# Optimization experiments

Hardware: AMD Instinct MI355X
Metric: run time of the kernel (lower is better)

## Reference

```python
import jax, jax.numpy as jnp
import numpy as np
import math

# Dims: d_model=192, expand=2 -> d_inner=d_ssm=384, headdim=64 -> nheads=6,
# d_state=128, K=4 scan directions, ngroups=1 (directions fused into state dim).
D_MODEL = 192
D_STATE = 128
D_CONV = 3
EXPAND = 2
HEADDIM = 64
CHUNK = 256
D_INNER = EXPAND * D_MODEL          # 384
D_SSM = D_INNER                     # default d_ssm (d_mlp == 0)
NHEADS = D_SSM // HEADDIM           # 6
K = 4                               # scan directions
HTOT = K * NHEADS                   # 24 heads in the fused scan
NSTATE = K * D_STATE                # 512 fused state dim (ngroups=1)
CONV_BC = 2 * D_STATE + NHEADS      # 262
B, H, W = 2, 64, 64


def _dwconv(x, w, b):
    # x: (B,C,H,W), w: (C,1,k,k) depthwise, SAME padding ((k-1)//2)
    y = jax.lax.conv_general_dilated(
        x, w, (1, 1), [(1, 1), (1, 1)],
        feature_group_count=x.shape[1],
        dimension_numbers=('NCHW', 'OIHW', 'NCHW'))
    return y + b[None, :, None, None]


def _ssd(x, dt_raw, A_logs, Bm, Cm, Ds, dt_bias):
    # Mamba2 chunked selective scan (dt_softplus=True, default dt_limit).
    # x: (b,l,h,p)  dt_raw: (b,l,h)  Bm,Cm: (b,l,n) with ngroups=1
    A = -jnp.exp(A_logs)                              # (h,)
    dt = jax.nn.softplus(dt_raw + dt_bias)            # (b,l,h)
    b, l, h, p = x.shape
    n = Bm.shape[-1]
    nc = l // CHUNK
    xc = x.reshape(b, nc, CHUNK, h, p)
    dtc = dt.reshape(b, nc, CHUNK, h)
    Bc = Bm.reshape(b, nc, CHUNK, n)
    Cc = Cm.reshape(b, nc, CHUNK, n)
    dA = dtc * A                                      # (b,nc,cs,h)
    acum = jnp.cumsum(dA, axis=2)
    # intra-chunk (causal, attention-like)
    a_t = jnp.transpose(acum, (0, 1, 3, 2))           # (b,nc,h,cs)
    diff = a_t[..., :, None] - a_t[..., None, :]      # (b,nc,h,i,j)
    causal = jnp.tril(jnp.ones((CHUNK, CHUNK), bool))
    Lmat = jnp.where(causal, jnp.exp(diff), 0.0)
    CB = jnp.einsum('bcin,bcjn->bcij', Cc, Bc)        # (b,nc,i,j)
    M = CB[:, :, None] * Lmat * jnp.transpose(dtc, (0, 1, 3, 2))[:, :, :, None, :]
    y = jnp.einsum('bchij,bcjhp->bcihp', M, xc)
    # chunk-final states
    decay_end = jnp.exp(acum[:, :, -1:, :] - acum)    # (b,nc,cs,h)
    states = jnp.einsum('bcjh,bcjn,bcjhp->bchpn', decay_end * dtc, Bc, xc)
    chunk_decay = jnp.exp(acum[:, :, -1, :])          # (b,nc,h)

    def step(S, inp):
        st, dec = inp
        return S * dec[:, :, None, None] + st, S

    S0 = jnp.zeros((b, h, p, n), x.dtype)
    _, prev = jax.lax.scan(step, S0, (jnp.moveaxis(states, 1, 0),
                                      jnp.moveaxis(chunk_decay, 1, 0)))
    prev = jnp.moveaxis(prev, 0, 1)                   # (b,nc,h,p,n)
    y = y + jnp.einsum('bcih,bcin,bchpn->bcihp', jnp.exp(acum), Cc, prev)
    y = y + xc * Ds[:, None]                          # D skip connection
    return y.reshape(b, l, h, p)


def _branch(u, u_cross, W_skip, W_xs, W_bcdt, conv_xs_w, conv_xs_b,
            conv_bc_w, conv_bc_b, dt_bias, A_logs, Ds, norm_w, W_out):
    Bb, Hh, Ww, _ = u.shape
    L = Hh * Ww
    z = (u @ W_skip).reshape(Bb, L, D_SSM)            # gate (d_mlp == 0)
    xs = jnp.transpose(u @ W_xs, (0, 3, 1, 2))        # (B,d_ssm,H,W)
    xs = jax.nn.silu(_dwconv(xs, conv_xs_w, conv_xs_b))
    bc = jnp.transpose(u_cross @ W_bcdt, (0, 3, 1, 2))
    bc = jax.nn.silu(_dwconv(bc, conv_bc_w, conv_bc_b))
    xbc = jnp.concatenate([xs, bc], axis=1)           # (B,646,H,W)
    C = xbc.shape[1]
    v = xbc.reshape(Bb, C, L)                         # HW raster
    vt = jnp.transpose(xbc, (0, 1, 3, 2)).reshape(Bb, C, L)  # WH raster
    hw = jnp.stack([v, vt], axis=1)                   # (B,2,C,L)
    xbcdt = jnp.concatenate([hw, jnp.flip(hw, axis=-1)], axis=1)  # (B,4,C,L)
    xp = xbcdt[:, :, :D_SSM]
    Bp = xbcdt[:, :, D_SSM:D_SSM + D_STATE]
    Cp = xbcdt[:, :, D_SSM + D_STATE:D_SSM + 2 * D_STATE]
    dtp = xbcdt[:, :, D_SSM + 2 * D_STATE:]
    x = xp.reshape(Bb, K * D_SSM, L).transpose(0, 2, 1).reshape(Bb, L, HTOT, HEADDIM)
    Bm = Bp.reshape(Bb, NSTATE, L).transpose(0, 2, 1)
    Cm = Cp.reshape(Bb, NSTATE, L).transpose(0, 2, 1)
    dt = dtp.reshape(Bb, HTOT, L).transpose(0, 2, 1)
    y = _ssd(x, dt, A_logs, Bm, Cm, Ds, dt_bias)      # (B,L,24,64)
    y = y.reshape(Bb, L, K, D_SSM)
    out_y = y[:, :, 0]
    inv_y = jnp.flip(y[:, :, 2:4], axis=1)            # (B,L,2,d_ssm)
    wh_y = y[:, :, 1].reshape(Bb, Ww, Hh, D_SSM).transpose(0, 2, 1, 3).reshape(Bb, L, D_SSM)
    invwh_y = inv_y[:, :, 1].reshape(Bb, Ww, Hh, D_SSM).transpose(0, 2, 1, 3).reshape(Bb, L, D_SSM)
    yf = out_y + inv_y[:, :, 0] + wh_y + invwh_y
    # gated RMSNorm (norm_before_gate=False, group_size == d_ssm)
    g = yf * jax.nn.silu(z)
    g = g * jax.lax.rsqrt(jnp.mean(g * g, axis=-1, keepdims=True) + 1e-5) * norm_w
    return (g @ W_out).reshape(Bb, Hh, Ww, D_MODEL)


def setup_inputs():
    key = jax.random.key(0)
    ks = jax.random.split(key, 16)
    f = lambda i, s: jax.random.normal(ks[i], s, jnp.float32)
    sc = 0.02
    dt = jnp.exp(jax.random.uniform(ks[10], (NHEADS,)) *
                 (math.log(0.1) - math.log(0.001)) + math.log(0.001))
    dt = jnp.maximum(dt, 1e-4)
    inv_dt = dt + jnp.log(-jnp.expm1(-dt))
    A = jax.random.uniform(ks[11], (NHEADS,), minval=1.0, maxval=16.0)
    return {
        'u1': f(0, (B, H, W, D_MODEL)),
        'u2': f(1, (B, H, W, D_MODEL)),
        'u2_cat_u1': f(2, (B, H, W, D_MODEL)),
        'u1_cat_u2': f(3, (B, H, W, D_MODEL)),
        'W_skip': f(4, (D_MODEL, D_SSM)) * sc,
        'W_xs': f(5, (D_MODEL, D_SSM)) * sc,
        'W_bcdt': f(6, (D_MODEL, CONV_BC)) * sc,
        'conv_xs_w': f(7, (D_SSM, 1, D_CONV, D_CONV)) * sc,
        'conv_xs_b': jnp.zeros((D_SSM,), jnp.float32),
        'conv_bc_w': f(8, (CONV_BC, 1, D_CONV, D_CONV)) * sc,
        'conv_bc_b': jnp.zeros((CONV_BC,), jnp.float32),
        'dt_bias': jnp.tile(inv_dt, K),
        'A_logs': jnp.tile(jnp.log(A), K),
        'Ds': jnp.ones((HTOT,), jnp.float32),
        'norm_w': jnp.ones((D_SSM,), jnp.float32),
        'W_out': f(9, (D_SSM, D_MODEL)) * sc,
    }


def reference(u1, u2, u2_cat_u1, u1_cat_u2, W_skip, W_xs, W_bcdt,
              conv_xs_w, conv_xs_b, conv_bc_w, conv_bc_b,
              dt_bias, A_logs, Ds, norm_w, W_out):
    args = (W_skip, W_xs, W_bcdt, conv_xs_w, conv_xs_b, conv_bc_w,
            conv_bc_b, dt_bias, A_logs, Ds, norm_w, W_out)
    out1 = _branch(u1, u2_cat_u1, *args)
    out2 = _branch(u2, u1_cat_u2, *args)
    return out1, out2
```

## Files before the change

### kernel.cpp

```cpp
#include <hip/hip_runtime.h>
#include <hip/hip_bf16.h>

#define DEV __device__ __forceinline__

static constexpr int LL   = 4096;
static constexpr int GG   = 4;
static constexpr int CBC  = 262;

typedef float f32x4  __attribute__((ext_vector_type(4)));
typedef short bf16x8 __attribute__((ext_vector_type(8)));
typedef short bf16x4v __attribute__((ext_vector_type(4)));
typedef short bf16x2 __attribute__((ext_vector_type(2)));

DEV int map_l(int s, int k) {
    int m = (k & 2) ? (4095 - s) : s;
    if (k & 1) m = ((m & 63) << 6) | (m >> 6);
    return m;
}
DEV float silu_f(float x) { return x / (1.f + __expf(-x)); }
DEV short f2bf(float f) {
    union { __hip_bfloat16 h; short s; } u;
    u.h = __float2bfloat16(f);
    return u.s;
}
DEV float bf2f(short s) {
    return __uint_as_float(((unsigned)(unsigned short)s) << 16);
}
DEV bf16x8 pack8(float4 a, float4 b) {
    bf16x8 r;
    r[0]=f2bf(a.x); r[1]=f2bf(a.y); r[2]=f2bf(a.z); r[3]=f2bf(a.w);
    r[4]=f2bf(b.x); r[5]=f2bf(b.y); r[6]=f2bf(b.z); r[7]=f2bf(b.w);
    return r;
}
DEV bf16x8 load8u(const __hip_bfloat16* p) {
    bf16x4v lo = *(const bf16x4v*)p;
    bf16x4v hi = *(const bf16x4v*)(p + 4);
    bf16x8 r;
    r[0]=lo[0]; r[1]=lo[1]; r[2]=lo[2]; r[3]=lo[3];
    r[4]=hi[0]; r[5]=hi[1]; r[6]=hi[2]; r[7]=hi[3];
    return r;
}
DEV void store16(__hip_bfloat16* p, const float* v) {
    bf16x8 a, b;
    #pragma unroll
    for (int e = 0; e < 8; ++e) { a[e] = f2bf(v[e]); b[e] = f2bf(v[8+e]); }
    *(bf16x8*)p = a;
    *((bf16x8*)p + 1) = b;
}
DEV void storeT(float v, float* p) { *p = v; }
DEV void storeT(float v, __hip_bfloat16* p) { *p = __float2bfloat16(v); }

__global__ void sentinel_k(float* out) { out[0] = 1e30f; }

__global__ void wt_all_k(const float* __restrict__ W_skip, const float* __restrict__ W_xs,
                         const float* __restrict__ W_bcdt, const float* __restrict__ W_out,
                         const float* __restrict__ norm_w, __hip_bfloat16* __restrict__ Wt)
{
    int idx = blockIdx.x * 256 + threadIdx.x;
    if (idx < 73728) {
        int n = idx / 192, k = idx - n * 192;
        Wt[idx] = __float2bfloat16(W_skip[(size_t)k * 384 + n]);
    } else if (idx < 147456) {
        int r = idx - 73728;
        int n = r / 192, k = r - n * 192;
        Wt[idx] = __float2bfloat16(W_xs[(size_t)k * 384 + n]);
    } else if (idx < 208896) {
        int r = idx - 147456;
        int n = r / 192, k = r - n * 192;
        Wt[idx] = __float2bfloat16(n < 262 ? W_bcdt[(size_t)k * 262 + n] : 0.f);
    } else if (idx < 282624) {
        int r = idx - 208896;
        int n = r / 384, k = r - n * 384;
        Wt[idx] = __float2bfloat16(W_out[(size_t)k * 192 + n] * norm_w[k]);
    }
}

template<int MODE, typename AT, typename OutT>
DEV void mgemm_body(const AT* __restrict__ A0, const AT* __restrict__ A1,
                    const __hip_bfloat16* __restrict__ Wt, OutT* __restrict__ C,
                    OutT* __restrict__ C2, int N, int Kd, int i0, int j0)
{
    int t = threadIdx.x;
    int w = t >> 6, lane = t & 63;
    int lr = lane & 15, kq = lane >> 4;
    const AT* arow[2];
    #pragma unroll
    for (int a = 0; a < 2; ++a) {
        int grow = i0 + w * 32 + a * 16 + lr;
        const AT* Ap = (grow < 8192) ? A0 : A1;
        arow[a] = Ap + (size_t)(grow & 8191) * Kd;
    }
    f32x4 acc[2][4] = {};
    for (int k0 = 0; k0 < Kd; k0 += 32) {
        int kb = k0 + kq * 8;
        bf16x8 af[2];
        #pragma unroll
        for (int a = 0; a < 2; ++a) {
            if constexpr (sizeof(AT) == 4)
                af[a] = pack8(*(const float4*)(arow[a] + kb), *(const float4*)(arow[a] + kb + 4));
            else
                af[a] = *(const bf16x8*)(arow[a] + kb);
        }
        #pragma unroll
        for (int b = 0; b < 4; ++b) {
            int n = j0 + b * 16 + lr;
            bf16x8 bfr = *(const bf16x8*)(Wt + (size_t)n * Kd + kb);
            #pragma unroll
            for (int a = 0; a < 2; ++a)
                acc[a][b] = __builtin_amdgcn_mfma_f32_16x16x32_bf16(af[a], bfr, acc[a][b], 0, 0, 0);
        }
    }
    #pragma unroll
    for (int a = 0; a < 2; ++a)
        #pragma unroll
        for (int b = 0; b < 4; ++b)
            #pragma unroll
            for (int r = 0; r < 4; ++r) {
                int row = i0 + w * 32 + a * 16 + kq * 4 + r;
                int col = j0 + b * 16 + lr;
                float v = acc[a][b][r];
                if constexpr (MODE == 0) {
                    if (col < N) storeT(v, &C[(size_t)row * N + col]);
                } else if constexpr (MODE == 1) {
                    if (col < N) storeT(silu_f(v), &C[(size_t)row * N + col]);
                } else {
                    if (col < 384) storeT(silu_f(v), &C[(size_t)row * 384 + col]);
                    else           storeT(v, &C2[(size_t)row * 384 + col - 384]);
                }
            }
}

__global__ __launch_bounds__(256) void mgemm_in_k(
    const float* __restrict__ u1, const float* __restrict__ u2,
    const float* __restrict__ u21, const float* __restrict__ u12,
    const __hip_bfloat16* __restrict__ Wt_skip, const __hip_bfloat16* __restrict__ Wt_bcdt,
    __hip_bfloat16* __restrict__ z_silu, __hip_bfloat16* __restrict__ pre_xs,
    __hip_bfloat16* __restrict__ pre_bc)
{
    int bid = blockIdx.x;
    if (bid < 1536) {
        mgemm_body<2, float, __hip_bfloat16>(u1, u2, Wt_skip, z_silu, pre_xs,
                                             768, 192, (bid / 12) * 128, (bid % 12) * 64);
    } else {
        int b = bid - 1536;
        mgemm_body<0, float, __hip_bfloat16>(u21, u12, Wt_bcdt, pre_bc, nullptr,
                                             CBC, 192, (b / 5) * 128, (b % 5) * 64);
    }
}

template<int STRIDE>
DEV void conv16(const __hip_bfloat16* __restrict__ pre, const float* __restrict__ cw,
                const float* __restrict__ cbia, int g, int h0, int w0, int chb,
                float* smem, float (*wsm)[9], float* bsm, int t)
{
    if (t < 144) wsm[t / 9][t % 9] = cw[(chb + t / 9) * 9 + t % 9];
    if (t < 16)  bsm[t] = cbia[chb + t];
    for (int i = t; i < 18 * 18 * 8; i += 256) {
        int cp = i & 7;
        int hw = i >> 3;
        int ww2 = hw % 18, hh = hw / 18;
        int gh = h0 - 1 + hh, gw = w0 - 1 + ww2;
        float v0 = 0.f, v1 = 0.f;
        if ((unsigned)gh < 64u && (unsigned)gw < 64u) {
            bf16x2 pv = *(const bf16x2*)(pre + ((size_t)g * LL + gh * 64 + gw) * STRIDE + chb + cp * 2);
            v0 = bf2f(pv[0]); v1 = bf2f(pv[1]);
        }
        smem[(hh * 18 + ww2) * 17 + cp * 2]     = v0;
        smem[(hh * 18 + ww2) * 17 + cp * 2 + 1] = v1;
    }
    __syncthreads();
    int h = t >> 4, w2 = t & 15;
    float out[16];
    #pragma unroll
    for (int ch = 0; ch < 16; ++ch) {
        float acc = bsm[ch];
        #pragma unroll
        for (int dy = 0; dy < 3; ++dy)
            #pragma unroll
            for (int dx = 0; dx < 3; ++dx)
                acc += smem[((h + dy) * 18 + (w2 + dx)) * 17 + ch] * wsm[ch][dy * 3 + dx];
        out[ch] = silu_f(acc);
    }
    __syncthreads();
    #pragma unroll
    for (int ch = 0; ch < 16; ++ch)
        smem[(h * 17 + w2) * 17 + ch] = out[ch];
    __syncthreads();
}

__global__ __launch_bounds__(256) void prep_k(
    const __hip_bfloat16* __restrict__ pre_bc, const float* __restrict__ cbw,
    const float* __restrict__ cbb, const __hip_bfloat16* __restrict__ pre_xs,
    const float* __restrict__ cxw, const float* __restrict__ cxb,
    const float* __restrict__ dt_bias, const float* __restrict__ A_logs,
    __hip_bfloat16* __restrict__ Bt, __hip_bfloat16* __restrict__ Cs,
    __hip_bfloat16* __restrict__ Bs, __hip_bfloat16* __restrict__ XtG,
    float* __restrict__ dt_arr, float* __restrict__ ac_arr,
    float* __restrict__ cdecay)
{
    __shared__ float smem[18 * 18 * 17];
    __shared__ float wsm[16][9];
    __shared__ float bsm[16];
    __shared__ float wsum[4];
    int bid = blockIdx.x;
    int t = threadIdx.x;
    if (bid < 2048) {
        int nt = bid & 31;
        int rest = bid >> 5;
        int wt = rest & 3, ht2 = (rest >> 2) & 3, g = rest >> 4;
        int h0 = ht2 * 16, w0 = wt * 16;
        int kd = nt >> 3, ch0 = (nt & 7) * 16;
        conv16<262>(pre_bc, cbw, cbb, g, h0, w0, ch0, smem, wsm, bsm, t);
        int pc = t >> 4, q = t & 15;
        int n = nt * 16 + pc;
        __hip_bfloat16* rowp = Bt + ((size_t)g * 512 + n) * 4096;
        float v[16];
        if (kd == 0) {
            #pragma unroll
            for (int e = 0; e < 16; ++e) v[e] = smem[(q * 17 + e) * 17 + pc];
            store16(rowp + (h0 + q) * 64 + w0, v);
        } else if (kd == 1) {
            #pragma unroll
            for (int e = 0; e < 16; ++e) v[e] = smem[(e * 17 + q) * 17 + pc];
            store16(rowp + (w0 + q) * 64 + h0, v);
        } else if (kd == 2) {
            #pragma unroll
            for (int e = 0; e < 16; ++e) v[e] = smem[(q * 17 + 15 - e) * 17 + pc];
            store16(rowp + 4095 - (h0 + q) * 64 - w0 - 15, v);
        } else {
            #pragma unroll
            for (int e = 0; e < 16; ++e) v[e] = smem[((15 - e) * 17 + q) * 17 + pc];
            store16(rowp + 4095 - (w0 + q) * 64 - h0 - 15, v);
        }
    } else if (bid < 4096) {
        int b2 = bid - 2048;
        int ct = b2 & 31;
        int rest = b2 >> 5;
        int wt = rest & 3, ht2 = (rest >> 2) & 3, g = rest >> 4;
        int h0 = ht2 * 16, w0 = wt * 16;
        bool isB = ct >= 16;
        int ctl = ct & 15;
        int kd = ctl >> 3, ch0 = (ctl & 7) * 16;
        int chb = (isB ? 0 : 128) + ch0;
        conv16<262>(pre_bc, cbw, cbb, g, h0, w0, chb, smem, wsm, bsm, t);
        __hip_bfloat16* dst = isB ? Bs : Cs;
        int h = t >> 4, w2 = t & 15;
        int s = (kd == 0) ? (h0 + h) * 64 + (w0 + w2) : (w0 + w2) * 64 + (h0 + h);
        float v[16];
        #pragma unroll
        for (int e = 0; e < 16; ++e) v[e] = smem[(h * 17 + w2) * 17 + e];
        store16(dst + ((size_t)g * 4096 + s) * 256 + kd * 128 + ch0, v);
    } else if (bid < 5632) {
        int b3 = bid - 4096;
        int ht = b3 % 24;
        int gc = b3 / 24;
        int c = gc & 15, g = gc >> 4;
        int k = ht / 6, h = ht % 6;
        int s = c * 256 + t;
        int l = map_l(s, k);
        int ch = 256 + h;
        float acc = cbb[ch];
        int hh0 = l >> 6, ww0 = l & 63;
        #pragma unroll
        for (int dy = 0; dy < 3; ++dy) {
            int gh = hh0 + dy - 1;
            if ((unsigned)gh >= 64u) continue;
            #pragma unroll
            for (int dx = 0; dx < 3; ++dx) {
                int gw = ww0 + dx - 1;
                if ((unsigned)gw >= 64u) continue;
                acc += __bfloat162float(pre_bc[((size_t)g * LL + gh * 64 + gw) * 262 + ch]) *
                       cbw[ch * 9 + dy * 3 + dx];
            }
        }
        float raw = silu_f(acc) + dt_bias[ht];
        float dtv = raw > 20.f ? raw : log1pf(__expf(raw));
        float dA = dtv * (-__expf(A_logs[ht]));
        float v = dA;
        #pragma unroll
        for (int off = 1; off < 64; off <<= 1) {
            float u = __shfl_up(v, off);
            if ((t & 63) >= off) v += u;
        }
        if ((t & 63) == 63) wsum[t >> 6] = v;
        __syncthreads();
        float add = 0.f;
        #pragma unroll
        for (int w2 = 0; w2 < 3; ++w2)
            if (w2 < (t >> 6)) add += wsum[w2];
        float cum = v + add;
        size_t base = ((size_t)g * 24 + ht) * LL + s;
        dt_arr[base] = dtv;
        ac_arr[base] = cum;
        if (t == 255) cdecay[(g * 24 + ht) * 16 + c] = __expf(cum);
    } else {
        int b4 = bid - 5632;
        int pct = b4 % 24;
        int rest = b4 / 24;
        int wt = rest & 3, ht2 = (rest >> 2) & 3, g = rest >> 4;
        int h0 = ht2 * 16, w0 = wt * 16, pc0 = pct * 16;
        conv16<384>(pre_xs, cxw, cxb, g, h0, w0, pc0, smem, wsm, bsm, t);
        int pc = t >> 4, q = t & 15;
        float v[16];
        size_t rowbase;
        #pragma unroll
        for (int e = 0; e < 16; ++e) v[e] = smem[(q * 17 + e) * 17 + pc];
        rowbase = ((size_t)(g * 2 + 0) * 384 + pc0 + pc) * 4096;
        store16(XtG + rowbase + (h0 + q) * 64 + w0, v);
        #pragma unroll
        for (int e = 0; e < 16; ++e) v[e] = smem[(e * 17 + q) * 17 + pc];
        rowbase = ((size_t)(g * 2 + 1) * 384 + pc0 + pc) * 4096;
        store16(XtG + rowbase + (w0 + q) * 64 + h0, v);
    }
}

__global__ __launch_bounds__(256) void cbst_k(
    const __hip_bfloat16* __restrict__ Cs, const __hip_bfloat16* __restrict__ Bs,
    __hip_bfloat16* __restrict__ CBm,
    const __hip_bfloat16* __restrict__ XtG, const __hip_bfloat16* __restrict__ Bt,
    const float* __restrict__ dt_arr, const float* __restrict__ ac_arr,
    __hip_bfloat16* __restrict__ states)
{
    __shared__ float wsh[256];
    __shared__ short xw[64][264];
    int bid = blockIdx.x;
    int t = threadIdx.x;
    int w = t >> 6, lane = t & 63;
    int lr = lane & 15, kq = lane >> 4;
    if (bid < 256) {
        int jq = bid & 3;
        int gc = bid >> 2;
        int c = gc & 15, g = gc >> 4;
        const __hip_bfloat16* cg = Cs + (size_t)g * 4096 * 256;
        const __hip_bfloat16* bsg = Bs + (size_t)g * 4096 * 256;
        f32x4 acc[4][4] = {};
        for (int ks = 0; ks < 16; ++ks) {
            int n0 = ks * 32 + kq * 8;
            int kd = n0 >> 7, nn = n0 & 127;
            int col = ((kd & 1) << 7) + nn;
            bf16x8 bfr[4];
            #pragma unroll
            for (int jt = 0; jt < 4; ++jt) {
                int j = jq * 64 + jt * 16 + lr;
                int s = c * 256 + j;
                int row = (kd < 2) ? s : 4095 - s;
                bfr[jt] = *(const bf16x8*)(bsg + (size_t)row * 256 + col);
            }
            #pragma unroll
            for (int iq = 0; iq < 4; ++iq) {
                int i = (w * 4 + iq) * 16 + lr;
                int s = c * 256 + i;
                int row = (kd < 2) ? s : 4095 - s;
                bf16x8 af = *(const bf16x8*)(cg + (size_t)row * 256 + col);
                #pragma unroll
                for (int jt = 0; jt < 4; ++jt)
                    acc[iq][jt] = __builtin_amdgcn_mfma_f32_16x16x32_bf16(af, bfr[jt], acc[iq][jt], 0, 0, 0);
            }
        }
        __hip_bfloat16* ob = CBm + (size_t)gc * 65536;
        #pragma unroll
        for (int iq = 0; iq < 4; ++iq)
            #pragma unroll
            for (int jt = 0; jt < 4; ++jt)
                #pragma unroll
                for (int r = 0; r < 4; ++r) {
                    int i = (w * 4 + iq) * 16 + kq * 4 + r;
                    int j = jq * 64 + jt * 16 + lr;
                    ob[(size_t)i * 256 + j] = __float2bfloat16(acc[iq][jt][r]);
                }
        return;
    }
    int sb = bid - 256;
    int task = (sb & 7) * 384 + (sb >> 3);
    int ht = task % 24;
    int rest = task / 24;
    int nh = rest & 1;
    int gc = rest >> 1;
    int c = gc & 15, g = gc >> 4;
    int kd = ht / 6;
    bool rev = kd >= 2;
    int c0 = (ht % 6) * 64;
    int n0 = nh * 256;
    const float* dtp = dt_arr + ((size_t)g * 24 + ht) * LL + c * 256;
    const float* acp = ac_arr + ((size_t)g * 24 + ht) * LL + c * 256;
    float ac_last = acp[255];
    wsh[t] = __expf(ac_last - acp[t]) * dtp[t];
    __syncthreads();
    const __hip_bfloat16* xg = XtG + ((size_t)(g * 2 + (kd & 1)) * 384 + c0) * 4096;
    #pragma unroll
    for (int r8 = 0; r8 < 8; ++r8) {
        int id = t + 256 * r8;
        int p = id >> 5;
        int jc = (id & 31) * 8;
        bf16x8 xv;
        if (!rev) {
            xv = *(const bf16x8*)(xg + (size_t)p * 4096 + c * 256 + jc);
        } else {
            bf16x8 tmp = load8u(xg + (size_t)p * 4096 + 4088 - c * 256 - jc);
            #pragma unroll
            for (int e = 0; e < 8; ++e) xv[e] = tmp[7 - e];
        }
        bf16x8 o;
        #pragma unroll
        for (int e = 0; e < 8; ++e) o[e] = f2bf(bf2f(xv[e]) * wsh[jc + e]);
        *(bf16x8*)&xw[p][jc] = o;
    }
    __syncthreads();
    const __hip_bfloat16* btg = Bt + ((size_t)g * 512 + n0) * 4096;
    f32x4 acc[4][4] = {};
    for (int ks = 0; ks < 8; ++ks) {
        int j0 = ks * 32 + kq * 8;
        bf16x8 af[4];
        #pragma unroll
        for (int pt = 0; pt < 4; ++pt)
            af[pt] = *(const bf16x8*)&xw[pt * 16 + lr][j0];
        #pragma unroll
        for (int nt = 0; nt < 4; ++nt) {
            int nl = (w * 4 + nt) * 16 + lr;
            bf16x8 bv = *(const bf16x8*)(btg + (size_t)nl * 4096 + c * 256 + j0);
            #pragma unroll
            for (int pt = 0; pt < 4; ++pt)
                acc[pt][nt] = __builtin_amdgcn_mfma_f32_16x16x32_bf16(af[pt], bv, acc[pt][nt], 0, 0, 0);
        }
    }
    __hip_bfloat16* ob = states + ((size_t)gc * 24 + ht) * 32768 + n0;
    #pragma unroll
    for (int pt = 0; pt < 4; ++pt)
        #pragma unroll
        for (int nt = 0; nt < 4; ++nt)
            #pragma unroll
            for (int r = 0; r < 4; ++r) {
                int p = pt * 16 + kq * 4 + r;
                int nl = (w * 4 + nt) * 16 + lr;
                ob[(size_t)p * 512 + nl] = __float2bfloat16(acc[pt][nt][r]);
            }
}

__global__ void scan_k(__hip_bfloat16* __restrict__ states, const float* __restrict__ cdecay)
{
    int idx = blockIdx.x * 256 + threadIdx.x;
    int g = idx / 98304;
    int r = idx - g * 98304;
    int ht = r >> 12;
    int pn8 = (r & 4095) * 8;
    const float* cd = cdecay + (g * 24 + ht) * 16;
    __hip_bfloat16* base = states + ((size_t)g * 384 + ht) * 32768 + pn8;
    float S[8] = {};
    #pragma unroll
    for (int c2 = 0; c2 < 16; ++c2) {
        bf16x8* p = (bf16x8*)(base + (size_t)c2 * 786432);
        bf16x8 tmp = *p;
        bf16x8 o;
        float dec = cd[c2];
        #pragma unroll
        for (int e = 0; e < 8; ++e) {
            o[e] = f2bf(S[e]);
            S[e] = S[e] * dec + bf2f(tmp[e]);
        }
        *p = o;
    }
}

__global__ __launch_bounds__(256) void yk(
    const __hip_bfloat16* __restrict__ XtG, const __hip_bfloat16* __restrict__ Cs,
    const __hip_bfloat16* __restrict__ CBm, const __hip_bfloat16* __restrict__ prev,
    const float* __restrict__ dt_arr, const float* __restrict__ ac_arr,
    const float* __restrict__ Ds, __hip_bfloat16* __restrict__ y4)
{
    __shared__ float acs[256], dts[256], ejdt[256];
    __shared__ short xl[64][264];
    int task = (blockIdx.x & 7) * 192 + (blockIdx.x >> 3);
    int ht = task % 24;
    int gc = task / 24;
    int c = gc & 15, g = gc >> 4;
    int kd = ht / 6;
    bool rev = kd >= 2;
    int c0 = (ht % 6) * 64;
    int t = threadIdx.x;
    int w = t >> 6, lane = t & 63;
    int lr = lane & 15, kq = lane >> 4;
    size_t abase = ((size_t)g * 24 + ht) * LL + c * 256;
    float ac_own = ac_arr[abase + t];
    float dt_own = dt_arr[abase + t];
    acs[t] = ac_own;
    dts[t] = dt_own;
    float acb0 = __shfl(ac_own, (t & 63) & ~31);
    ejdt[t] = __expf(acb0 - ac_own) * dt_own;
    const __hip_bfloat16* xg = XtG + ((size_t)(g * 2 + (kd & 1)) * 384 + c0) * 4096;
    #pragma unroll
    for (int r8 = 0; r8 < 8; ++r8) {
        int id = t + 256 * r8;
        int p = id >> 5;
        int jc = (id & 31) * 8;
        bf16x8 xv;
        if (!rev) {
            xv = *(const bf16x8*)(xg + (size_t)p * 4096 + c * 256 + jc);
        } else {
            bf16x8 tmp = load8u(xg + (size_t)p * 4096 + 4088 - c * 256 - jc);
            #pragma unroll
            for (int e = 0; e < 8; ++e) xv[e] = tmp[7 - e];
        }
        *(bf16x8*)&xl[p][jc] = xv;
    }
    __syncthreads();
    const __hip_bfloat16* cbb = CBm + (size_t)gc * 65536;
    const __hip_bfloat16* cg = Cs + (size_t)g * 4096 * 256;
    f32x4 acc[4][4] = {};
    const __hip_bfloat16* pv = prev + ((size_t)gc * 24 + ht) * 32768;
    auto ld2 = [&](int ns, bf16x8* afq, bf16x8* pb) {
        int n0 = ns * 32 + kq * 8;
        int kd2 = n0 >> 7, nn = n0 & 127;
        int col = ((kd2 & 1) << 7) + nn;
        #pragma unroll
        for (int q = 0; q < 4; ++q) {
            int i = (w + 4 * q) * 16 + lr;
            int s = c * 256 + i;
            int row = (kd2 < 2) ? s : 4095 - s;
            afq[q] = *(const bf16x8*)(cg + (size_t)row * 256 + col);
        }
        #pragma unroll
        for (int pt = 0; pt < 4; ++pt)
            pb[pt] = *(const bf16x8*)(pv + (size_t)(pt * 16 + lr) * 512 + n0);
    };
    auto fma2 = [&](bf16x8* afq, bf16x8* pb) {
        #pragma unroll
        for (int q = 0; q < 4; ++q)
            #pragma unroll
            for (int pt = 0; pt < 4; ++pt)
                acc[q][pt] = __builtin_amdgcn_mfma_f32_16x16x32_bf16(afq[q], pb[pt], acc[q][pt], 0, 0, 0);
    };
    {
        bf16x8 afA[4], pbA[4], afB[4], pbB[4];
        ld2(0, afA, pbA);
        #pragma unroll
        for (int ns = 0; ns < 16; ns += 2) {
            if (ns + 1 < 16) ld2(ns + 1, afB, pbB);
            fma2(afA, pbA);
            if (ns + 2 < 16) ld2(ns + 2, afA, pbA);
            fma2(afB, pbB);
        }
    }
    #pragma unroll
    for (int q = 0; q < 4; ++q)
        #pragma unroll
        for (int r = 0; r < 4; ++r) {
            float er = __expf(acs[(w + 4 * q) * 16 + kq * 4 + r]);
            #pragma unroll
            for (int pt = 0; pt < 4; ++pt) acc[q][pt][r] *= er;
        }
    float aci_q[4];
    #pragma unroll
    for (int q = 0; q < 4; ++q) aci_q[q] = acs[(w + 4 * q) * 16 + lr];
    for (int ks = 0; ks < 8; ++ks) {
        int j0 = ks * 32 + kq * 8;
        bf16x8 xb[4];
        #pragma unroll
        for (int pt = 0; pt < 4; ++pt)
            xb[pt] = *(const bf16x8*)&xl[pt * 16 + lr][j0];
        float acb = acs[ks * 32];
        float ej[8];
        #pragma unroll
        for (int e = 0; e < 8; ++e) ej[e] = ejdt[j0 + e];
        #pragma unroll
        for (int q = 0; q < 4; ++q) {
            int rt = w + 4 * q;
            if (rt < 2 * ks) continue;
            int i = rt * 16 + lr;
            float r2 = __expf(aci_q[q] - acb);
            bf16x8 cb8 = *(const bf16x8*)(cbb + (size_t)i * 256 + j0);
            bf16x8 af;
            if (rt >= 2 * ks + 2) {
                #pragma unroll
                for (int e = 0; e < 8; ++e)
                    af[e] = f2bf(r2 * ej[e] * bf2f(cb8[e]));
            } else {
                #pragma unroll
                for (int e = 0; e < 8; ++e) {
                    float coef = r2 * ej[e] * bf2f(cb8[e]);
                    af[e] = (j0 + e <= i) ? f2bf(coef) : (short)0;
                }
            }
            #pragma unroll
            for (int pt = 0; pt < 4; ++pt)
                acc[q][pt] = __builtin_amdgcn_mfma_f32_16x16x32_bf16(af, xb[pt], acc[q][pt], 0, 0, 0);
        }
    }
    float Dsv = Ds[ht];
    __hip_bfloat16* yb = y4 + (((size_t)(g * 4 + kd) * 4096 + c * 256) * 384) + c0;
    #pragma unroll
    for (int q = 0; q < 4; ++q) {
        int rt = w + 4 * q;
        #pragma unroll
        for (int pt = 0; pt < 4; ++pt) {
            int p = pt * 16 + lr;
            int ibase = rt * 16 + kq * 4;
            bf16x4v x4 = *(const bf16x4v*)&xl[p][ibase];
            #pragma unroll
            for (int r = 0; r < 4; ++r) {
                int i = ibase + r;
                float xv = bf2f(x4[r]);
                yb[(size_t)i * 384 + p] = __float2bfloat16(acc[q][pt][r] + Dsv * xv);
            }
        }
    }
}

__global__ __launch_bounds__(256) void gateout_k(
    const __hip_bfloat16* __restrict__ y4, const __hip_bfloat16* __restrict__ z_silu,
    const __hip_bfloat16* __restrict__ Wt_out, float* __restrict__ out)
{
    __shared__ short gnl[32][392];
    int b = blockIdx.x;
    int t = threadIdx.x;
    int row0 = b * 32;
    {
        int rloc = t >> 3, part = t & 7;
        int row = row0 + rloc;
        int g = row >> 12, l = row & 4095;
        int Tl = ((l & 63) << 6) | (l >> 6);
        const __hip_bfloat16* p0 = y4 + ((size_t)(g * 4 + 0) * 4096 + l) * 384;
        const __hip_bfloat16* p1 = y4 + ((size_t)(g * 4 + 1) * 4096 + Tl) * 384;
        const __hip_bfloat16* p2 = y4 + ((size_t)(g * 4 + 2) * 4096 + 4095 - l) * 384;
        const __hip_bfloat16* p3 = y4 + ((size_t)(g * 4 + 3) * 4096 + 4095 - Tl) * 384;
        const __hip_bfloat16* zp = z_silu + ((size_t)g * LL + l) * 384;
        int cb = part * 48;
        float vf[48];
        float ssq = 0.f;
        #pragma unroll
        for (int cg = 0; cg < 6; ++cg) {
            int cc = cb + cg * 8;
            bf16x8 a0 = *(const bf16x8*)(p0 + cc);
            bf16x8 a1 = *(const bf16x8*)(p1 + cc);
            bf16x8 a2 = *(const bf16x8*)(p2 + cc);
            bf16x8 a3 = *(const bf16x8*)(p3 + cc);
            bf16x8 zv = *(const bf16x8*)(zp + cc);
            #pragma unroll
            for (int e = 0; e < 8; ++e) {
                float yf = bf2f(a0[e]) + bf2f(a1[e]) + bf2f(a2[e]) + bf2f(a3[e]);
                float v = yf * bf2f(zv[e]);
                vf[cg * 8 + e] = v;
                ssq += v * v;
            }
        }
        ssq += __shfl_xor(ssq, 1);
        ssq += __shfl_xor(ssq, 2);
        ssq += __shfl_xor(ssq, 4);
        float rs = rsqrtf(ssq * (1.f / 384.f) + 1e-5f);
        #pragma unroll
        for (int cg = 0; cg < 6; ++cg) {
            bf16x8 o;
            #pragma unroll
            for (int e = 0; e < 8; ++e) o[e] = f2bf(vf[cg * 8 + e] * rs);
            *(bf16x8*)&gnl[rloc][cb + cg * 8] = o;
        }
    }
    __syncthreads();
    int w = t >> 6, lane = t & 63;
    int lr = lane & 15, kq = lane >> 4;
    int rowTile = w >> 1, colHalf = w & 1;
    f32x4 acc[6] = {};
    for (int k0 = 0; k0 < 384; k0 += 32) {
        int kb = k0 + kq * 8;
        bf16x8 af = *(const bf16x8*)&gnl[rowTile * 16 + lr][kb];
        #pragma unroll
        for (int b2 = 0; b2 < 6; ++b2) {
            int n = colHalf * 96 + b2 * 16 + lr;
            bf16x8 bfr = *(const bf16x8*)(Wt_out + (size_t)n * 384 + kb);
            acc[b2] = __builtin_amdgcn_mfma_f32_16x16x32_bf16(af, bfr, acc[b2], 0, 0, 0);
        }
    }
    #pragma unroll
    for (int b2 = 0; b2 < 6; ++b2)
        #pragma unroll
        for (int r = 0; r < 4; ++r) {
            int row = row0 + rowTile * 16 + kq * 4 + r;
            int col = colHalf * 96 + b2 * 16 + lr;
            out[(size_t)row * 192 + col] = acc[b2][r];
        }
}

extern "C" void kernel_launch(void* const* d_in, const int* in_sizes, int n_in,
                              void* d_out, int out_size, void* d_ws, size_t ws_size,
                              hipStream_t stream)
{
    const float* u1      = (const float*)d_in[0];
    const float* u2      = (const float*)d_in[1];
    const float* u21     = (const float*)d_in[2];
    const float* u12     = (const float*)d_in[3];
    const float* W_skip  = (const float*)d_in[4];
    const float* W_xs    = (const float*)d_in[5];
    const float* W_bcdt  = (const float*)d_in[6];
    const float* cxw     = (const float*)d_in[7];
    const float* cxb     = (const float*)d_in[8];
    const float* cbw     = (const float*)d_in[9];
    const float* cbb     = (const float*)d_in[10];
    const float* dt_bias = (const float*)d_in[11];
    const float* A_logs  = (const float*)d_in[12];
    const float* Ds      = (const float*)d_in[13];
    const float* norm_w  = (const float*)d_in[14];
    const float* W_out   = (const float*)d_in[15];
    float* out = (float*)d_out;

    char* w = (char*)d_ws;
    size_t o_y4  = 0;
    size_t o_st  = o_y4 + 50331648;
    size_t o_z   = o_st + 100663296;
    size_t o_xtg = o_z  + 12582912;
    size_t o_bt  = o_xtg + 25165824;
    size_t o_cs  = o_bt + 16777216;
    size_t o_cbm = o_cs + 8388608;
    size_t o_dt  = o_cbm + 8388608;
    size_t o_ac  = o_dt + 1572864;
    size_t o_cd  = o_ac + 1572864;
    size_t o_wt  = o_cd + 8192;
    size_t o_bs  = o_wt + 589824;
    size_t total = o_bs + 8388608;
    if (total > ws_size) {
        sentinel_k<<<1, 1, 0, stream>>>(out);
        return;
    }
    __hip_bfloat16* y4     = (__hip_bfloat16*)(w + o_y4);
    __hip_bfloat16* states = (__hip_bfloat16*)(w + o_st);
    __hip_bfloat16* z_silu = (__hip_bfloat16*)(w + o_z);
    __hip_bfloat16* XtG    = (__hip_bfloat16*)(w + o_xtg);
    __hip_bfloat16* Bt     = (__hip_bfloat16*)(w + o_bt);
    __hip_bfloat16* Cs     = (__hip_bfloat16*)(w + o_cs);
    __hip_bfloat16* CBm    = (__hip_bfloat16*)(w + o_cbm);
    float*          dt_arr = (float*)(w + o_dt);
    float*          ac_arr = (float*)(w + o_ac);
    float*          cdecay = (float*)(w + o_cd);
    __hip_bfloat16* Wt     = (__hip_bfloat16*)(w + o_wt);
    __hip_bfloat16* Bs     = (__hip_bfloat16*)(w + o_bs);
    __hip_bfloat16* Wt_skip = Wt;
    __hip_bfloat16* Wt_bcdt = Wt + 147456;
    __hip_bfloat16* Wt_out  = Wt + 208896;
    __hip_bfloat16* pre_bc = (__hip_bfloat16*)(w + o_st);
    __hip_bfloat16* pre_xs = (__hip_bfloat16*)(w + o_st + 8650752);

    dim3 blk(256);
    wt_all_k<<<dim3(1104), blk, 0, stream>>>(W_skip, W_xs, W_bcdt, W_out, norm_w, Wt);
    mgemm_in_k<<<dim3(2176), blk, 0, stream>>>(u1, u2, u21, u12, Wt_skip, Wt_bcdt,
                                               z_silu, pre_xs, pre_bc);
    prep_k<<<dim3(7168), blk, 0, stream>>>(pre_bc, cbw, cbb, pre_xs, cxw, cxb,
                                           dt_bias, A_logs, Bt, Cs, Bs, XtG,
                                           dt_arr, ac_arr, cdecay);
    cbst_k<<<dim3(3328), blk, 0, stream>>>(Cs, Bs, CBm, XtG, Bt, dt_arr, ac_arr, states);
    scan_k<<<dim3(1536), blk, 0, stream>>>(states, cdecay);
    yk<<<dim3(1536), blk, 0, stream>>>(XtG, Cs, CBm, states, dt_arr, ac_arr, Ds, y4);
    gateout_k<<<dim3(512), blk, 0, stream>>>(y4, z_silu, Wt_out, out);
}
```

Baseline: 401.8 us.

## Rewrite skip/xs input GEMM with 128x128 register-blocked MFMA tiles and XCD-aware block mapping

```diff
diff --git a/kernel.cpp b/kernel.cpp
--- a/kernel.cpp
+++ b/kernel.cpp
@@ -137,12 +137,49 @@
     __hip_bfloat16* __restrict__ z_silu, __hip_bfloat16* __restrict__ pre_xs,
     __hip_bfloat16* __restrict__ pre_bc)
 {
-    int bid = blockIdx.x;
-    if (bid < 1536) {
-        mgemm_body<2, float, __hip_bfloat16>(u1, u2, Wt_skip, z_silu, pre_xs,
-                                             768, 192, (bid / 12) * 128, (bid % 12) * 64);
+    int bid = (blockIdx.x & 7) * 176 + (blockIdx.x >> 3);
+    int t = threadIdx.x;
+    if (bid < 768) {
+        int i0 = (bid / 6) * 128, j0 = (bid % 6) * 128;
+        int w = t >> 6, lane = t & 63;
+        int lr = lane & 15, kq = lane >> 4;
+        const float* arow[2];
+        #pragma unroll
+        for (int a = 0; a < 2; ++a) {
+            int grow = i0 + w * 32 + a * 16 + lr;
+            const float* Ap = (grow < 8192) ? u1 : u2;
+            arow[a] = Ap + (size_t)(grow & 8191) * 192;
+        }
+        f32x4 acc[2][8] = {};
+        for (int k0 = 0; k0 < 192; k0 += 32) {
+            int kb = k0 + kq * 8;
+            bf16x8 af[2];
+            #pragma unroll
+            for (int a = 0; a < 2; ++a)
+                af[a] = pack8(*(const float4*)(arow[a] + kb), *(const float4*)(arow[a] + kb + 4));
+            #pragma unroll
+            for (int b = 0; b < 8; ++b) {
+                int n = j0 + b * 16 + lr;
+                bf16x8 bfr = *(const bf16x8*)(Wt_skip + (size_t)n * 192 + kb);
+                #pragma unroll
+                for (int a = 0; a < 2; ++a)
+                    acc[a][b] = __builtin_amdgcn_mfma_f32_16x16x32_bf16(af[a], bfr, acc[a][b], 0, 0, 0);
+            }
+        }
+        #pragma unroll
+        for (int a = 0; a < 2; ++a)
+            #pragma unroll
+            for (int b = 0; b < 8; ++b)
+                #pragma unroll
+                for (int r = 0; r < 4; ++r) {
+                    int row = i0 + w * 32 + a * 16 + kq * 4 + r;
+                    int col = j0 + b * 16 + lr;
+                    float v = acc[a][b][r];
+                    if (col < 384) storeT(silu_f(v), &z_silu[(size_t)row * 384 + col]);
+                    else           storeT(v, &pre_xs[(size_t)row * 384 + col - 384]);
+                }
     } else {
-        int b = bid - 1536;
+        int b = bid - 768;
         mgemm_body<0, float, __hip_bfloat16>(u21, u12, Wt_bcdt, pre_bc, nullptr,
                                              CBC, 192, (b / 5) * 128, (b % 5) * 64);
     }
@@ -739,7 +776,7 @@
 
     dim3 blk(256);
     wt_all_k<<<dim3(1104), blk, 0, stream>>>(W_skip, W_xs, W_bcdt, W_out, norm_w, Wt);
-    mgemm_in_k<<<dim3(2176), blk, 0, stream>>>(u1, u2, u21, u12, Wt_skip, Wt_bcdt,
+    mgemm_in_k<<<dim3(1408), blk, 0, stream>>>(u1, u2, u21, u12, Wt_skip, Wt_bcdt,
                                                z_silu, pre_xs, pre_bc);
     prep_k<<<dim3(7168), blk, 0, stream>>>(pre_bc, cbw, cbb, pre_xs, cxw, cxb,
                                            dt_bias, A_logs, Bt, Cs, Bs, XtG,
```

New measurement: 426.8 us. 1.06x slower.
